# Kernel tuning notes

Measured on AMD Instinct MI355X. Metric: run time of the kernel, lower is better.

The kernel has to match this reference:

```python
import jax, jax.numpy as jnp
import numpy as np

V, D, G, E, B, S = 50000, 300, 256, 1600000, 64, 64


def setup_inputs() -> dict:
    key = jax.random.key(0)
    k = jax.random.split(key, 6)
    emb = jax.random.normal(k[0], (V, D), jnp.float32) * 0.02
    emb = emb.at[0].set(0.0)  # padding_idx=0
    W1 = jax.random.normal(k[1], (D, G), jnp.float32) * (1.0 / np.sqrt(D))
    b1 = jnp.zeros((G,), jnp.float32)
    W2 = jax.random.normal(k[2], (G, G), jnp.float32) * (1.0 / np.sqrt(G))
    b2 = jnp.zeros((G,), jnp.float32)
    edge_index = jax.random.randint(k[3], (2, E), 0, V, dtype=jnp.int64)
    word_ids = jax.random.randint(k[4], (B, S), 0, V, dtype=jnp.int64)
    return {"emb": emb, "W1": W1, "b1": b1, "W2": W2, "b2": b2,
            "edge_index": edge_index, "word_ids": word_ids}


def _gcn_conv(x, W, b, src, dst, num_nodes):
    """PyG GCNConv: add self-loops, symmetric deg^{-1/2} normalization.
    out_i = sum_{j->i} h_j / sqrt(deg_j * deg_i) + h_i / deg_i + b,
    with deg_i = 1 (self-loop) + in-degree(i), h = x @ W."""
    h = x @ W                                        # (N, G)
    deg = jnp.ones((num_nodes,), h.dtype).at[dst].add(1.0)
    inv_sqrt = jax.lax.rsqrt(deg)                    # (N,)
    coef = inv_sqrt[src] * inv_sqrt[dst]             # (E,)
    agg = jnp.zeros_like(h).at[dst].add(h[src] * coef[:, None])
    agg = agg + h * (inv_sqrt * inv_sqrt)[:, None]   # self-loop term
    return agg + b


def reference(emb, W1, b1, W2, b2, edge_index, word_ids):
    num_nodes = emb.shape[0]
    src, dst = edge_index[0], edge_index[1]
    h = jax.nn.relu(_gcn_conv(emb, W1, b1, src, dst, num_nodes))  # (V, G)
    h = _gcn_conv(h, W2, b2, src, dst, num_nodes)                 # (V, G)
    return h[word_ids]                                            # (B, S, G)
```

## Files before the change

kernel.cpp:

```cpp
#include <hip/hip_runtime.h>
#include <hip/hip_bf16.h>

#define NV 50000
#define ND 300
#define NDP 320
#define NG 256
#define NE 1600000
#define NBS 4096
#define NBUCK 196
#define EPB 8192
#define CPAD 16
#define GEMM1_BLOCKS 782
#define PREP_W1 320
#define PREP_W2 256
#define PREP_HIST 1024

typedef short short8 __attribute__((ext_vector_type(8)));
typedef float f32x4 __attribute__((ext_vector_type(4)));
typedef float f32x2 __attribute__((ext_vector_type(2)));
typedef _Float16 half4 __attribute__((ext_vector_type(4)));

__device__ __forceinline__ ushort f2bf(float f) {
    unsigned u = __builtin_bit_cast(unsigned, f);
    unsigned r = (u + 0x7fffu + ((u >> 16) & 1u)) >> 16;
    return (ushort)r;
}
__device__ __forceinline__ float bf2f(ushort h) {
    unsigned u = ((unsigned)h) << 16;
    return __builtin_bit_cast(float, u);
}

__global__ __launch_bounds__(256) void prep_kernel(const float* __restrict__ W1,
                                                   const float* __restrict__ W2,
                                                   ushort* __restrict__ W1Th,
                                                   ushort* __restrict__ W1Tl,
                                                   ushort* __restrict__ W2Th,
                                                   ushort* __restrict__ W2Tl,
                                                   const int* __restrict__ dst,
                                                   int* __restrict__ bucket_count) {
    int t = threadIdx.x;
    if (blockIdx.x < PREP_W1) {
        int idx = blockIdx.x * 256 + t;
        int n = idx / NDP, k = idx - n * NDP;
        float v = (k < ND) ? W1[(size_t)k * NG + n] : 0.f;
        ushort h = f2bf(v);
        W1Th[idx] = h;
        W1Tl[idx] = f2bf(v - bf2f(h));
    } else if (blockIdx.x < PREP_W1 + PREP_W2) {
        int j = (blockIdx.x - PREP_W1) * 256 + t;
        int n = j / NG, k = j - n * NG;
        float v = W2[(size_t)k * NG + n];
        ushort h = f2bf(v);
        W2Th[j] = h;
        W2Tl[j] = f2bf(v - bf2f(h));
    } else {
        __shared__ int bh[NBUCK];
        for (int b = t; b < NBUCK; b += 256) bh[b] = 0;
        __syncthreads();
        int blk = blockIdx.x - (PREP_W1 + PREP_W2);
        for (int i = blk * 256 + t; i * 4 < NE; i += PREP_HIST * 256) {
            int4 d = *(const int4*)(dst + i * 4);
            atomicAdd(&bh[d.x >> 8], 1);
            atomicAdd(&bh[d.y >> 8], 1);
            atomicAdd(&bh[d.z >> 8], 1);
            atomicAdd(&bh[d.w >> 8], 1);
        }
        __syncthreads();
        for (int b = t; b < NBUCK; b += 256)
            if (bh[b]) atomicAdd(&bucket_count[b * CPAD], bh[b]);
    }
}

__global__ __launch_bounds__(256) void bucket_scan(const int* __restrict__ bucket_count,
                                                   int* __restrict__ bucket_base,
                                                   int* __restrict__ bucket_cursor) {
    __shared__ int s[256];
    int t = threadIdx.x;
    int v = (t < NBUCK) ? bucket_count[t * CPAD] : 0;
    s[t] = v;
    __syncthreads();
    for (int d = 1; d < 256; d <<= 1) {
        int x = (t >= d) ? s[t - d] : 0;
        __syncthreads();
        s[t] += x;
        __syncthreads();
    }
    int excl = s[t] - v;
    if (t < NBUCK) {
        bucket_base[t] = excl;
        bucket_cursor[t * CPAD] = excl;
    }
    if (t == 255) bucket_base[NBUCK] = s[255];
}

__global__ __launch_bounds__(256) void gemm1_scatter(const float* __restrict__ A,
                                                     const ushort* __restrict__ BTh,
                                                     unsigned char* __restrict__ C8,
                                                     const int* __restrict__ ei,
                                                     int* __restrict__ bucket_cursor,
                                                     unsigned* __restrict__ rec) {
    int t = threadIdx.x;
    if (blockIdx.x < GEMM1_BLOCKS) {
        __shared__ short Ah[128][40];
        __shared__ short Bh[128][40];
        const int lda = ND, ldb = NDP, M = NV, K = ND, KP = NDP;
        int bid = blockIdx.x;
        int bm = (bid >> 1) * 128;
        int bn = (bid & 1) * 128;
        int lane = t & 63, wv = t >> 6;
        int wm = (wv >> 1) * 64, wn = (wv & 1) * 64;
        int srow = t >> 1;
        int skq = (t & 1) * 16;
        f32x4 acc[4][4];
#pragma unroll
        for (int mi = 0; mi < 4; ++mi)
#pragma unroll
            for (int ni = 0; ni < 4; ++ni) acc[mi][ni] = (f32x4)0.0f;

        for (int k0 = 0; k0 < KP; k0 += 32) {
            int gk = k0 + skq;
            {
                int gr = bm + srow;
                short va[16];
                float v[16];
                if (gr < M && gk < K) {
                    if (gk + 16 <= K) {
#pragma unroll
                        for (int q = 0; q < 4; ++q) {
                            float4 p = *(const float4*)(A + (size_t)gr * lda + gk + q * 4);
                            v[q * 4 + 0] = p.x; v[q * 4 + 1] = p.y;
                            v[q * 4 + 2] = p.z; v[q * 4 + 3] = p.w;
                        }
                    } else {
#pragma unroll
                        for (int e = 0; e < 16; ++e)
                            v[e] = (gk + e < K) ? A[(size_t)gr * lda + gk + e] : 0.f;
                    }
                } else {
#pragma unroll
                    for (int e = 0; e < 16; ++e) v[e] = 0.f;
                }
#pragma unroll
                for (int e = 0; e < 16; ++e) va[e] = (short)f2bf(v[e]);
                *(short8*)&Ah[srow][skq] = *(short8*)&va[0];
                *(short8*)&Ah[srow][skq + 8] = *(short8*)&va[8];
            }
            {
                int nr = bn + srow;
                short8 bh0 = *(const short8*)(BTh + (size_t)nr * ldb + gk);
                short8 bh1 = *(const short8*)(BTh + (size_t)nr * ldb + gk + 8);
                *(short8*)&Bh[srow][skq] = bh0;
                *(short8*)&Bh[srow][skq + 8] = bh1;
            }
            __syncthreads();
            int m16 = lane & 15, kb = (lane >> 4) * 8;
            short8 a_h[4], b_h[4];
#pragma unroll
            for (int mi = 0; mi < 4; ++mi)
                a_h[mi] = *(const short8*)&Ah[wm + mi * 16 + m16][kb];
#pragma unroll
            for (int ni = 0; ni < 4; ++ni)
                b_h[ni] = *(const short8*)&Bh[wn + ni * 16 + m16][kb];
#pragma unroll
            for (int mi = 0; mi < 4; ++mi)
#pragma unroll
                for (int ni = 0; ni < 4; ++ni)
                    acc[mi][ni] = __builtin_amdgcn_mfma_f32_16x16x32_bf16(a_h[mi], b_h[ni], acc[mi][ni], 0, 0, 0);
            __syncthreads();
        }
        int m16 = lane & 15, rq = lane >> 4;
#pragma unroll
        for (int mi = 0; mi < 4; ++mi)
#pragma unroll
            for (int ni = 0; ni < 4; ++ni) {
                int row0 = bm + wm + mi * 16 + rq * 4;
                int col = bn + wn + ni * 16 + m16;
                int p01 = __builtin_amdgcn_cvt_pk_fp8_f32(acc[mi][ni][0], acc[mi][ni][1], 0, false);
                int p23 = __builtin_amdgcn_cvt_pk_fp8_f32(acc[mi][ni][2], acc[mi][ni][3], 0, false);
                if (row0 + 0 < M) C8[(size_t)(row0 + 0) * NG + col] = (unsigned char)(p01 & 0xff);
                if (row0 + 1 < M) C8[(size_t)(row0 + 1) * NG + col] = (unsigned char)((p01 >> 8) & 0xff);
                if (row0 + 2 < M) C8[(size_t)(row0 + 2) * NG + col] = (unsigned char)(p23 & 0xff);
                if (row0 + 3 < M) C8[(size_t)(row0 + 3) * NG + col] = (unsigned char)((p23 >> 8) & 0xff);
            }
    } else {
        __shared__ int cnt[NBUCK];
        __shared__ int basel[NBUCK];
        int e0 = (blockIdx.x - GEMM1_BLOCKS) * EPB;
        for (int b = t; b < NBUCK; b += 256) cnt[b] = 0;
        __syncthreads();
        for (int q = 0; q < EPB / 1024; ++q) {
            int i4 = e0 + q * 1024 + t * 4;
            if (i4 < NE) {
                int4 d = *(const int4*)(ei + NE + i4);
                atomicAdd(&cnt[d.x >> 8], 1);
                atomicAdd(&cnt[d.y >> 8], 1);
                atomicAdd(&cnt[d.z >> 8], 1);
                atomicAdd(&cnt[d.w >> 8], 1);
            }
        }
        __syncthreads();
        for (int b = t; b < NBUCK; b += 256) {
            int c = cnt[b];
            basel[b] = c ? atomicAdd(&bucket_cursor[b * CPAD], c) : 0;
        }
        __syncthreads();
        for (int b = t; b < NBUCK; b += 256) cnt[b] = 0;
        __syncthreads();
        for (int q = 0; q < EPB / 1024; ++q) {
            int i4 = e0 + q * 1024 + t * 4;
            if (i4 < NE) {
                int4 s = *(const int4*)(ei + i4);
                int4 d = *(const int4*)(ei + NE + i4);
                int b0 = d.x >> 8, b1 = d.y >> 8, b2 = d.z >> 8, b3 = d.w >> 8;
                int r0 = atomicAdd(&cnt[b0], 1);
                rec[basel[b0] + r0] = (unsigned)s.x | ((unsigned)(d.x & 255) << 16);
                int r1 = atomicAdd(&cnt[b1], 1);
                rec[basel[b1] + r1] = (unsigned)s.y | ((unsigned)(d.y & 255) << 16);
                int r2 = atomicAdd(&cnt[b2], 1);
                rec[basel[b2] + r2] = (unsigned)s.z | ((unsigned)(d.z & 255) << 16);
                int r3 = atomicAdd(&cnt[b3], 1);
                rec[basel[b3] + r3] = (unsigned)s.w | ((unsigned)(d.w & 255) << 16);
            }
        }
    }
}

__global__ __launch_bounds__(256) void csr_build(const unsigned* __restrict__ rec,
                                                 const int* __restrict__ bucket_base,
                                                 int* __restrict__ off,
                                                 float* __restrict__ inv_sqrt,
                                                 ushort* __restrict__ csr_src) {
    __shared__ int degl[256];
    __shared__ int s[256];
    int b = blockIdx.x, t = threadIdx.x;
    degl[t] = 0;
    __syncthreads();
    int r0 = bucket_base[b], r1 = bucket_base[b + 1];
    for (int i = r0 + t; i < r1; i += 256)
        atomicAdd(&degl[(rec[i] >> 16) & 255], 1);
    __syncthreads();
    int v = degl[t];
    s[t] = v;
    __syncthreads();
    for (int d = 1; d < 256; d <<= 1) {
        int x = (t >= d) ? s[t - d] : 0;
        __syncthreads();
        s[t] += x;
        __syncthreads();
    }
    int excl = s[t] - v + r0;
    int n = (b << 8) + t;
    if (n < NV) {
        off[n] = excl;
        inv_sqrt[n] = rsqrtf((float)(v + 1));
    }
    if (b == NBUCK - 1 && t == 0) off[NV] = NE;
    __syncthreads();
    degl[t] = excl;
    __syncthreads();
    for (int i = r0 + t; i < r1; i += 256) {
        unsigned e = rec[i];
        int p = atomicAdd(&degl[(e >> 16) & 255], 1);
        csr_src[p] = (ushort)(e & 0xffff);
    }
}

__global__ __launch_bounds__(256) void gemm_out(const float* __restrict__ A,
                                                int lda,
                                                const ushort* __restrict__ BTh,
                                                const ushort* __restrict__ BTl,
                                                int ldb,
                                                int M, int K, int KP,
                                                float* __restrict__ C32,
                                                const float* __restrict__ bias) {
    __shared__ short Ah[128][40];
    __shared__ short Bh[128][40];
    __shared__ short Bl[128][40];
    int t = threadIdx.x;
    int bm = blockIdx.x * 128;
    int bn = blockIdx.y * 128;
    int lane = t & 63, wv = t >> 6;
    int wm = (wv >> 1) * 64, wn = (wv & 1) * 64;
    int srow = t >> 1;
    int skq = (t & 1) * 16;
    f32x4 acc[4][4];
#pragma unroll
    for (int mi = 0; mi < 4; ++mi)
#pragma unroll
        for (int ni = 0; ni < 4; ++ni) acc[mi][ni] = (f32x4)0.0f;

    for (int k0 = 0; k0 < KP; k0 += 32) {
        int gk = k0 + skq;
        {
            int gr = bm + srow;
            short va[16];
            float v[16];
            if (gr < M && gk < K) {
#pragma unroll
                for (int q = 0; q < 4; ++q) {
                    float4 p = *(const float4*)(A + (size_t)gr * lda + gk + q * 4);
                    v[q * 4 + 0] = p.x; v[q * 4 + 1] = p.y;
                    v[q * 4 + 2] = p.z; v[q * 4 + 3] = p.w;
                }
            } else {
#pragma unroll
                for (int e = 0; e < 16; ++e) v[e] = 0.f;
            }
#pragma unroll
            for (int e = 0; e < 16; ++e) va[e] = (short)f2bf(v[e]);
            *(short8*)&Ah[srow][skq] = *(short8*)&va[0];
            *(short8*)&Ah[srow][skq + 8] = *(short8*)&va[8];
        }
        {
            int nr = bn + srow;
            short8 bh0 = *(const short8*)(BTh + (size_t)nr * ldb + gk);
            short8 bh1 = *(const short8*)(BTh + (size_t)nr * ldb + gk + 8);
            short8 bl0 = *(const short8*)(BTl + (size_t)nr * ldb + gk);
            short8 bl1 = *(const short8*)(BTl + (size_t)nr * ldb + gk + 8);
            *(short8*)&Bh[srow][skq] = bh0;
            *(short8*)&Bh[srow][skq + 8] = bh1;
            *(short8*)&Bl[srow][skq] = bl0;
            *(short8*)&Bl[srow][skq + 8] = bl1;
        }
        __syncthreads();
        int m16 = lane & 15, kb = (lane >> 4) * 8;
        short8 a_h[4], b_h[4], b_l[4];
#pragma unroll
        for (int mi = 0; mi < 4; ++mi)
            a_h[mi] = *(const short8*)&Ah[wm + mi * 16 + m16][kb];
#pragma unroll
        for (int ni = 0; ni < 4; ++ni) {
            b_h[ni] = *(const short8*)&Bh[wn + ni * 16 + m16][kb];
            b_l[ni] = *(const short8*)&Bl[wn + ni * 16 + m16][kb];
        }
#pragma unroll
        for (int mi = 0; mi < 4; ++mi)
#pragma unroll
            for (int ni = 0; ni < 4; ++ni) {
                acc[mi][ni] = __builtin_amdgcn_mfma_f32_16x16x32_bf16(a_h[mi], b_h[ni], acc[mi][ni], 0, 0, 0);
                acc[mi][ni] = __builtin_amdgcn_mfma_f32_16x16x32_bf16(a_h[mi], b_l[ni], acc[mi][ni], 0, 0, 0);
            }
        __syncthreads();
    }
    int m16 = lane & 15, rq = lane >> 4;
#pragma unroll
    for (int mi = 0; mi < 4; ++mi)
#pragma unroll
        for (int ni = 0; ni < 4; ++ni) {
#pragma unroll
            for (int r = 0; r < 4; ++r) {
                int row = bm + wm + mi * 16 + rq * 4 + r;
                int col = bn + wn + ni * 16 + m16;
                if (row < M)
                    C32[(size_t)row * NG + col] = acc[mi][ni][r] + bias[col];
            }
        }
}

__global__ __launch_bounds__(256) void agg1_kernel(const unsigned char* __restrict__ h1f8,
                                                   const int* __restrict__ off,
                                                   const ushort* __restrict__ csr_src,
                                                   const float* __restrict__ inv_sqrt,
                                                   const float* __restrict__ b1,
                                                   _Float16* __restrict__ x1) {
    int wv = threadIdx.x >> 6, lane = threadIdx.x & 63;
    int i = blockIdx.x * 4 + wv;
    if (i >= NV) return;
    int c4 = lane * 4;
    int s0 = off[i], s1 = off[i + 1];
    float a0 = 0.f, a1 = 0.f, a2 = 0.f, a3 = 0.f;
    int j = s0;
    for (; j + 16 <= s1; j += 16) {
        int sx[16];
        float wx[16];
        unsigned pk[16];
#pragma unroll
        for (int u = 0; u < 16; ++u) sx[u] = csr_src[j + u];
#pragma unroll
        for (int u = 0; u < 16; ++u) {
            wx[u] = inv_sqrt[sx[u]];
            pk[u] = *(const unsigned*)(h1f8 + (size_t)sx[u] * NG + c4);
        }
#pragma unroll
        for (int u = 0; u < 16; ++u) {
            f32x2 v01 = __builtin_amdgcn_cvt_pk_f32_fp8(pk[u], false);
            f32x2 v23 = __builtin_amdgcn_cvt_pk_f32_fp8(pk[u], true);
            a0 += wx[u] * v01[0];
            a1 += wx[u] * v01[1];
            a2 += wx[u] * v23[0];
            a3 += wx[u] * v23[1];
        }
    }
    for (; j + 4 <= s1; j += 4) {
        int sx[4];
        float wx[4];
        unsigned pk[4];
#pragma unroll
        for (int u = 0; u < 4; ++u) sx[u] = csr_src[j + u];
#pragma unroll
        for (int u = 0; u < 4; ++u) {
            wx[u] = inv_sqrt[sx[u]];
            pk[u] = *(const unsigned*)(h1f8 + (size_t)sx[u] * NG + c4);
        }
#pragma unroll
        for (int u = 0; u < 4; ++u) {
            f32x2 v01 = __builtin_amdgcn_cvt_pk_f32_fp8(pk[u], false);
            f32x2 v23 = __builtin_amdgcn_cvt_pk_f32_fp8(pk[u], true);
            a0 += wx[u] * v01[0];
            a1 += wx[u] * v01[1];
            a2 += wx[u] * v23[0];
            a3 += wx[u] * v23[1];
        }
    }
    for (; j < s1; ++j) {
        int s = csr_src[j];
        float w = inv_sqrt[s];
        unsigned pk = *(const unsigned*)(h1f8 + (size_t)s * NG + c4);
        f32x2 v01 = __builtin_amdgcn_cvt_pk_f32_fp8(pk, false);
        f32x2 v23 = __builtin_amdgcn_cvt_pk_f32_fp8(pk, true);
        a0 += w * v01[0];
        a1 += w * v01[1];
        a2 += w * v23[0];
        a3 += w * v23[1];
    }
    float is = inv_sqrt[i], is2 = is * is;
    unsigned pks = *(const unsigned*)(h1f8 + (size_t)i * NG + c4);
    f32x2 s01 = __builtin_amdgcn_cvt_pk_f32_fp8(pks, false);
    f32x2 s23 = __builtin_amdgcn_cvt_pk_f32_fp8(pks, true);
    float4 bb = *(const float4*)(b1 + c4);
    half4 o;
    o[0] = (_Float16)fmaxf(is * a0 + s01[0] * is2 + bb.x, 0.f);
    o[1] = (_Float16)fmaxf(is * a1 + s01[1] * is2 + bb.y, 0.f);
    o[2] = (_Float16)fmaxf(is * a2 + s23[0] * is2 + bb.z, 0.f);
    o[3] = (_Float16)fmaxf(is * a3 + s23[1] * is2 + bb.w, 0.f);
    *(half4*)(x1 + (size_t)i * NG + c4) = o;
}

__global__ __launch_bounds__(256) void agg2_kernel(const _Float16* __restrict__ x1,
                                                   const int* __restrict__ off,
                                                   const ushort* __restrict__ csr_src,
                                                   const float* __restrict__ inv_sqrt,
                                                   const int* __restrict__ word_ids,
                                                   float* __restrict__ y) {
    int wv = threadIdx.x >> 6, lane = threadIdx.x & 63;
    int p = blockIdx.x * 4 + wv;
    if (p >= NBS) return;
    int n = word_ids[p];
    int c4 = lane * 4;
    int s0 = off[n], s1 = off[n + 1];
    float a0 = 0.f, a1 = 0.f, a2 = 0.f, a3 = 0.f;
    int j = s0;
    for (; j + 16 <= s1; j += 16) {
        int sx[16];
        float wx[16];
        half4 vx[16];
#pragma unroll
        for (int u = 0; u < 16; ++u) sx[u] = csr_src[j + u];
#pragma unroll
        for (int u = 0; u < 16; ++u) {
            wx[u] = inv_sqrt[sx[u]];
            vx[u] = *(const half4*)(x1 + (size_t)sx[u] * NG + c4);
        }
#pragma unroll
        for (int u = 0; u < 16; ++u) {
            a0 += wx[u] * (float)vx[u][0];
            a1 += wx[u] * (float)vx[u][1];
            a2 += wx[u] * (float)vx[u][2];
            a3 += wx[u] * (float)vx[u][3];
        }
    }
    for (; j + 4 <= s1; j += 4) {
        int sx[4];
        float wx[4];
        half4 vx[4];
#pragma unroll
        for (int u = 0; u < 4; ++u) sx[u] = csr_src[j + u];
#pragma unroll
        for (int u = 0; u < 4; ++u) {
            wx[u] = inv_sqrt[sx[u]];
            vx[u] = *(const half4*)(x1 + (size_t)sx[u] * NG + c4);
        }
#pragma unroll
        for (int u = 0; u < 4; ++u) {
            a0 += wx[u] * (float)vx[u][0];
            a1 += wx[u] * (float)vx[u][1];
            a2 += wx[u] * (float)vx[u][2];
            a3 += wx[u] * (float)vx[u][3];
        }
    }
    for (; j < s1; ++j) {
        int s = csr_src[j];
        float w = inv_sqrt[s];
        half4 hv = *(const half4*)(x1 + (size_t)s * NG + c4);
        a0 += w * (float)hv[0];
        a1 += w * (float)hv[1];
        a2 += w * (float)hv[2];
        a3 += w * (float)hv[3];
    }
    float is = inv_sqrt[n], is2 = is * is;
    half4 sv = *(const half4*)(x1 + (size_t)n * NG + c4);
    float4 o;
    o.x = is * a0 + (float)sv[0] * is2;
    o.y = is * a1 + (float)sv[1] * is2;
    o.z = is * a2 + (float)sv[2] * is2;
    o.w = is * a3 + (float)sv[3] * is2;
    *(float4*)(y + (size_t)p * NG + c4) = o;
}

extern "C" void kernel_launch(void* const* d_in, const int* in_sizes, int n_in,
                              void* d_out, int out_size, void* d_ws, size_t ws_size,
                              hipStream_t stream) {
    const float* emb = (const float*)d_in[0];
    const float* W1  = (const float*)d_in[1];
    const float* b1  = (const float*)d_in[2];
    const float* W2  = (const float*)d_in[3];
    const float* b2  = (const float*)d_in[4];
    const int*   ei  = (const int*)d_in[5];
    const int*   wid = (const int*)d_in[6];
    float* out = (float*)d_out;

    char* w = (char*)d_ws;
    auto alloc = [&](size_t bytes) {
        void* p = (void*)w;
        w += (bytes + 255) & ~(size_t)255;
        return p;
    };
    int*    off      = (int*)alloc((size_t)(NV + 1) * 4);
    float*  inv_sqrt = (float*)alloc((size_t)NV * 4);
    int*    bucket_count  = (int*)alloc((size_t)NBUCK * CPAD * 4);
    int*    bucket_base   = (int*)alloc((size_t)(NBUCK + 1) * 4);
    int*    bucket_cursor = (int*)alloc((size_t)NBUCK * CPAD * 4);
    ushort* csr_src  = (ushort*)alloc((size_t)NE * 2);
    unsigned* bucket_rec = (unsigned*)alloc((size_t)NE * 4);
    ushort* W1T_h    = (ushort*)alloc((size_t)NG * NDP * 2);
    ushort* W1T_l    = (ushort*)alloc((size_t)NG * NDP * 2);
    ushort* W2T_h    = (ushort*)alloc((size_t)NG * NG * 2);
    ushort* W2T_l    = (ushort*)alloc((size_t)NG * NG * 2);
    unsigned char* h1f8 = (unsigned char*)alloc((size_t)NV * NG);
    _Float16* x1     = (_Float16*)alloc((size_t)NV * NG * 2);
    float*  y        = (float*)alloc((size_t)NBS * NG * 4);

    hipMemsetAsync(bucket_count, 0, (size_t)NBUCK * CPAD * 4, stream);

    prep_kernel<<<PREP_W1 + PREP_W2 + PREP_HIST, 256, 0, stream>>>(
        W1, W2, W1T_h, W1T_l, W2T_h, W2T_l, ei + NE, bucket_count);
    bucket_scan<<<1, 256, 0, stream>>>(bucket_count, bucket_base, bucket_cursor);
    gemm1_scatter<<<GEMM1_BLOCKS + NBUCK, 256, 0, stream>>>(emb, W1T_h, h1f8,
                                                            ei, bucket_cursor, bucket_rec);
    csr_build<<<NBUCK, 256, 0, stream>>>(bucket_rec, bucket_base, off, inv_sqrt, csr_src);

    agg1_kernel<<<(NV + 3) / 4, 256, 0, stream>>>(h1f8, off, csr_src, inv_sqrt, b1, x1);
    agg2_kernel<<<(NBS + 3) / 4, 256, 0, stream>>>(x1, off, csr_src, inv_sqrt, wid, y);
    {
        dim3 grid((NBS + 127) / 128, NG / 128);
        gemm_out<<<grid, 256, 0, stream>>>(y, NG, W2T_h, W2T_l, NG,
                                           NBS, NG, NG, out, b2);
    }
}
```

Measured before the change: 191.5 us.

## Slice feature matrices into 32-column planes and aggregate per slice with lane groups

Hidden features h1 (fp8) and x1 (fp16) are now stored as eight column slices of 32 features each, with every slice contiguous over nodes. The aggregation kernels give each block one slice and split a wave into 8 edge groups of 8 lanes, then combine the groups with xor shuffles. The aim is to shrink each slice's working set so gathered rows stay in cache, and to run 8 edges in parallel per wave. The edge-scatter blocks are also placed ahead of the GEMM blocks with smaller per-block edge counts so they start early. The risks are extra shuffle reductions, 8x more blocks re-reading the CSR indices, and GEMM output stores that are scattered in the sliced layout.

```diff
diff --git a/kernel.cpp b/kernel.cpp
--- a/kernel.cpp
+++ b/kernel.cpp
@@ -8,7 +8,8 @@
 #define NE 1600000
 #define NBS 4096
 #define NBUCK 196
-#define EPB 8192
+#define EPB 4096
+#define SCAT_BLOCKS 391
 #define CPAD 16
 #define GEMM1_BLOCKS 782
 #define PREP_W1 320
@@ -95,97 +96,15 @@
 
 __global__ __launch_bounds__(256) void gemm1_scatter(const float* __restrict__ A,
                                                      const ushort* __restrict__ BTh,
-                                                     unsigned char* __restrict__ C8,
+                                                     unsigned char* __restrict__ h1s,
                                                      const int* __restrict__ ei,
                                                      int* __restrict__ bucket_cursor,
                                                      unsigned* __restrict__ rec) {
     int t = threadIdx.x;
-    if (blockIdx.x < GEMM1_BLOCKS) {
-        __shared__ short Ah[128][40];
-        __shared__ short Bh[128][40];
-        const int lda = ND, ldb = NDP, M = NV, K = ND, KP = NDP;
-        int bid = blockIdx.x;
-        int bm = (bid >> 1) * 128;
-        int bn = (bid & 1) * 128;
-        int lane = t & 63, wv = t >> 6;
-        int wm = (wv >> 1) * 64, wn = (wv & 1) * 64;
-        int srow = t >> 1;
-        int skq = (t & 1) * 16;
-        f32x4 acc[4][4];
-#pragma unroll
-        for (int mi = 0; mi < 4; ++mi)
-#pragma unroll
-            for (int ni = 0; ni < 4; ++ni) acc[mi][ni] = (f32x4)0.0f;
-
-        for (int k0 = 0; k0 < KP; k0 += 32) {
-            int gk = k0 + skq;
-            {
-                int gr = bm + srow;
-                short va[16];
-                float v[16];
-                if (gr < M && gk < K) {
-                    if (gk + 16 <= K) {
-#pragma unroll
-                        for (int q = 0; q < 4; ++q) {
-                            float4 p = *(const float4*)(A + (size_t)gr * lda + gk + q * 4);
-                            v[q * 4 + 0] = p.x; v[q * 4 + 1] = p.y;
-                            v[q * 4 + 2] = p.z; v[q * 4 + 3] = p.w;
-                        }
-                    } else {
-#pragma unroll
-                        for (int e = 0; e < 16; ++e)
-                            v[e] = (gk + e < K) ? A[(size_t)gr * lda + gk + e] : 0.f;
-                    }
-                } else {
-#pragma unroll
-                    for (int e = 0; e < 16; ++e) v[e] = 0.f;
-                }
-#pragma unroll
-                for (int e = 0; e < 16; ++e) va[e] = (short)f2bf(v[e]);
-                *(short8*)&Ah[srow][skq] = *(short8*)&va[0];
-                *(short8*)&Ah[srow][skq + 8] = *(short8*)&va[8];
-            }
-            {
-                int nr = bn + srow;
-                short8 bh0 = *(const short8*)(BTh + (size_t)nr * ldb + gk);
-                short8 bh1 = *(const short8*)(BTh + (size_t)nr * ldb + gk + 8);
-                *(short8*)&Bh[srow][skq] = bh0;
-                *(short8*)&Bh[srow][skq + 8] = bh1;
-            }
-            __syncthreads();
-            int m16 = lane & 15, kb = (lane >> 4) * 8;
-            short8 a_h[4], b_h[4];
-#pragma unroll
-            for (int mi = 0; mi < 4; ++mi)
-                a_h[mi] = *(const short8*)&Ah[wm + mi * 16 + m16][kb];
-#pragma unroll
-            for (int ni = 0; ni < 4; ++ni)
-                b_h[ni] = *(const short8*)&Bh[wn + ni * 16 + m16][kb];
-#pragma unroll
-            for (int mi = 0; mi < 4; ++mi)
-#pragma unroll
-                for (int ni = 0; ni < 4; ++ni)
-                    acc[mi][ni] = __builtin_amdgcn_mfma_f32_16x16x32_bf16(a_h[mi], b_h[ni], acc[mi][ni], 0, 0, 0);
-            __syncthreads();
-        }
-        int m16 = lane & 15, rq = lane >> 4;
-#pragma unroll
-        for (int mi = 0; mi < 4; ++mi)
-#pragma unroll
-            for (int ni = 0; ni < 4; ++ni) {
-                int row0 = bm + wm + mi * 16 + rq * 4;
-                int col = bn + wn + ni * 16 + m16;
-                int p01 = __builtin_amdgcn_cvt_pk_fp8_f32(acc[mi][ni][0], acc[mi][ni][1], 0, false);
-                int p23 = __builtin_amdgcn_cvt_pk_fp8_f32(acc[mi][ni][2], acc[mi][ni][3], 0, false);
-                if (row0 + 0 < M) C8[(size_t)(row0 + 0) * NG + col] = (unsigned char)(p01 & 0xff);
-                if (row0 + 1 < M) C8[(size_t)(row0 + 1) * NG + col] = (unsigned char)((p01 >> 8) & 0xff);
-                if (row0 + 2 < M) C8[(size_t)(row0 + 2) * NG + col] = (unsigned char)(p23 & 0xff);
-                if (row0 + 3 < M) C8[(size_t)(row0 + 3) * NG + col] = (unsigned char)((p23 >> 8) & 0xff);
-            }
-    } else {
+    if (blockIdx.x < SCAT_BLOCKS) {
         __shared__ int cnt[NBUCK];
         __shared__ int basel[NBUCK];
-        int e0 = (blockIdx.x - GEMM1_BLOCKS) * EPB;
+        int e0 = blockIdx.x * EPB;
         for (int b = t; b < NBUCK; b += 256) cnt[b] = 0;
         __syncthreads();
         for (int q = 0; q < EPB / 1024; ++q) {
@@ -222,6 +141,89 @@
                 rec[basel[b3] + r3] = (unsigned)s.w | ((unsigned)(d.w & 255) << 16);
             }
         }
+    } else {
+        __shared__ short Ah[128][40];
+        __shared__ short Bh[128][40];
+        const int lda = ND, ldb = NDP, M = NV, K = ND, KP = NDP;
+        int bid = blockIdx.x - SCAT_BLOCKS;
+        int bm = (bid >> 1) * 128;
+        int bn = (bid & 1) * 128;
+        int lane = t & 63, wv = t >> 6;
+        int wm = (wv >> 1) * 64, wn = (wv & 1) * 64;
+        int srow = t >> 1;
+        int skq = (t & 1) * 16;
+        f32x4 acc[4][4];
+#pragma unroll
+        for (int mi = 0; mi < 4; ++mi)
+#pragma unroll
+            for (int ni = 0; ni < 4; ++ni) acc[mi][ni] = (f32x4)0.0f;
+
+        for (int k0 = 0; k0 < KP; k0 += 32) {
+            int gk = k0 + skq;
+            {
+                int gr = bm + srow;
+                short va[16];
+                float v[16];
+                if (gr < M && gk < K) {
+                    if (gk + 16 <= K) {
+#pragma unroll
+                        for (int q = 0; q < 4; ++q) {
+                            float4 p = *(const float4*)(A + (size_t)gr * lda + gk + q * 4);
+                            v[q * 4 + 0] = p.x; v[q * 4 + 1] = p.y;
+                            v[q * 4 + 2] = p.z; v[q * 4 + 3] = p.w;
+                        }
+                    } else {
+#pragma unroll
+                        for (int e = 0; e < 16; ++e)
+                            v[e] = (gk + e < K) ? A[(size_t)gr * lda + gk + e] : 0.f;
+                    }
+                } else {
+#pragma unroll
+                    for (int e = 0; e < 16; ++e) v[e] = 0.f;
+                }
+#pragma unroll
+                for (int e = 0; e < 16; ++e) va[e] = (short)f2bf(v[e]);
+                *(short8*)&Ah[srow][skq] = *(short8*)&va[0];
+                *(short8*)&Ah[srow][skq + 8] = *(short8*)&va[8];
+            }
+            {
+                int nr = bn + srow;
+                short8 bh0 = *(const short8*)(BTh + (size_t)nr * ldb + gk);
+                short8 bh1 = *(const short8*)(BTh + (size_t)nr * ldb + gk + 8);
+                *(short8*)&Bh[srow][skq] = bh0;
+                *(short8*)&Bh[srow][skq + 8] = bh1;
+            }
+            __syncthreads();
+            int m16 = lane & 15, kb = (lane >> 4) * 8;
+            short8 a_h[4], b_h[4];
+#pragma unroll
+            for (int mi = 0; mi < 4; ++mi)
+                a_h[mi] = *(const short8*)&Ah[wm + mi * 16 + m16][kb];
+#pragma unroll
+            for (int ni = 0; ni < 4; ++ni)
+                b_h[ni] = *(const short8*)&Bh[wn + ni * 16 + m16][kb];
+#pragma unroll
+            for (int mi = 0; mi < 4; ++mi)
+#pragma unroll
+                for (int ni = 0; ni < 4; ++ni)
+                    acc[mi][ni] = __builtin_amdgcn_mfma_f32_16x16x32_bf16(a_h[mi], b_h[ni], acc[mi][ni], 0, 0, 0);
+            __syncthreads();
+        }
+        int m16 = lane & 15, rq = lane >> 4;
+#pragma unroll
+        for (int mi = 0; mi < 4; ++mi)
+#pragma unroll
+            for (int ni = 0; ni < 4; ++ni) {
+                int row0 = bm + wm + mi * 16 + rq * 4;
+                int col = bn + wn + ni * 16 + m16;
+                size_t base = (size_t)(col >> 5) * NV * 32 + (col & 31);
+                int p01 = __builtin_amdgcn_cvt_pk_fp8_f32(acc[mi][ni][0], acc[mi][ni][1], 0, false);
+                int p23 = __builtin_amdgcn_cvt_pk_fp8_f32(acc[mi][ni][2], acc[mi][ni][3], 0, false);
+                if (row0 + 0 < M) h1s[base + (size_t)(row0 + 0) * 32] = (unsigned char)(p01 & 0xff);
+                if (row0 + 1 < M) h1s[base + (size_t)(row0 + 1) * 32] = (unsigned char)((p01 >> 8) & 0xff);
+                if (row0 + 2 < M) h1s[base + (size_t)(row0 + 2) * 32] = (unsigned char)(p23 & 0xff);
+                if (row0 + 3 < M) h1s[base + (size_t)(row0 + 3) * 32] = (unsigned char)((p23 >> 8) & 0xff);
+            }
     }
 }
 
@@ -357,154 +359,133 @@
         }
 }
 
-__global__ __launch_bounds__(256) void agg1_kernel(const unsigned char* __restrict__ h1f8,
+__global__ __launch_bounds__(256) void agg1_kernel(const unsigned char* __restrict__ h1s,
                                                    const int* __restrict__ off,
                                                    const ushort* __restrict__ csr_src,
                                                    const float* __restrict__ inv_sqrt,
                                                    const float* __restrict__ b1,
-                                                   _Float16* __restrict__ x1) {
+                                                   _Float16* __restrict__ x1s) {
     int wv = threadIdx.x >> 6, lane = threadIdx.x & 63;
-    int i = blockIdx.x * 4 + wv;
-    if (i >= NV) return;
-    int c4 = lane * 4;
-    int s0 = off[i], s1 = off[i + 1];
-    float a0 = 0.f, a1 = 0.f, a2 = 0.f, a3 = 0.f;
-    int j = s0;
-    for (; j + 16 <= s1; j += 16) {
-        int sx[16];
-        float wx[16];
-        unsigned pk[16];
-#pragma unroll
-        for (int u = 0; u < 16; ++u) sx[u] = csr_src[j + u];
-#pragma unroll
-        for (int u = 0; u < 16; ++u) {
-            wx[u] = inv_sqrt[sx[u]];
-            pk[u] = *(const unsigned*)(h1f8 + (size_t)sx[u] * NG + c4);
-        }
-#pragma unroll
-        for (int u = 0; u < 16; ++u) {
-            f32x2 v01 = __builtin_amdgcn_cvt_pk_f32_fp8(pk[u], false);
-            f32x2 v23 = __builtin_amdgcn_cvt_pk_f32_fp8(pk[u], true);
-            a0 += wx[u] * v01[0];
-            a1 += wx[u] * v01[1];
-            a2 += wx[u] * v23[0];
-            a3 += wx[u] * v23[1];
-        }
-    }
-    for (; j + 4 <= s1; j += 4) {
-        int sx[4];
-        float wx[4];
-        unsigned pk[4];
-#pragma unroll
-        for (int u = 0; u < 4; ++u) sx[u] = csr_src[j + u];
-#pragma unroll
-        for (int u = 0; u < 4; ++u) {
-            wx[u] = inv_sqrt[sx[u]];
-            pk[u] = *(const unsigned*)(h1f8 + (size_t)sx[u] * NG + c4);
-        }
-#pragma unroll
-        for (int u = 0; u < 4; ++u) {
-            f32x2 v01 = __builtin_amdgcn_cvt_pk_f32_fp8(pk[u], false);
-            f32x2 v23 = __builtin_amdgcn_cvt_pk_f32_fp8(pk[u], true);
-            a0 += wx[u] * v01[0];
-            a1 += wx[u] * v01[1];
-            a2 += wx[u] * v23[0];
-            a3 += wx[u] * v23[1];
-        }
-    }
-    for (; j < s1; ++j) {
-        int s = csr_src[j];
-        float w = inv_sqrt[s];
-        unsigned pk = *(const unsigned*)(h1f8 + (size_t)s * NG + c4);
-        f32x2 v01 = __builtin_amdgcn_cvt_pk_f32_fp8(pk, false);
-        f32x2 v23 = __builtin_amdgcn_cvt_pk_f32_fp8(pk, true);
-        a0 += w * v01[0];
-        a1 += w * v01[1];
-        a2 += w * v23[0];
-        a3 += w * v23[1];
-    }
-    float is = inv_sqrt[i], is2 = is * is;
-    unsigned pks = *(const unsigned*)(h1f8 + (size_t)i * NG + c4);
-    f32x2 s01 = __builtin_amdgcn_cvt_pk_f32_fp8(pks, false);
-    f32x2 s23 = __builtin_amdgcn_cvt_pk_f32_fp8(pks, true);
-    float4 bb = *(const float4*)(b1 + c4);
-    half4 o;
-    o[0] = (_Float16)fmaxf(is * a0 + s01[0] * is2 + bb.x, 0.f);
-    o[1] = (_Float16)fmaxf(is * a1 + s01[1] * is2 + bb.y, 0.f);
-    o[2] = (_Float16)fmaxf(is * a2 + s23[0] * is2 + bb.z, 0.f);
-    o[3] = (_Float16)fmaxf(is * a3 + s23[1] * is2 + bb.w, 0.f);
-    *(half4*)(x1 + (size_t)i * NG + c4) = o;
-}
-
-__global__ __launch_bounds__(256) void agg2_kernel(const _Float16* __restrict__ x1,
+    int slice = blockIdx.x & 7;
+    int chunk = blockIdx.x >> 3;
+    int g = lane >> 3, p = lane & 7;
+    const unsigned char* hb = h1s + (size_t)slice * NV * 32;
+    _Float16* xb = x1s + (size_t)slice * NV * 32;
+    float4 bb = *(const float4*)(b1 + slice * 32 + p * 4);
+    for (int q = 0; q < 4; ++q) {
+        int i = chunk * 16 + wv * 4 + q;
+        if (i >= NV) break;
+        int s0 = off[i], s1 = off[i + 1];
+        float a0 = 0.f, a1 = 0.f, a2 = 0.f, a3 = 0.f;
+        int j = s0;
+        for (; j + 16 <= s1; j += 16) {
+            int sA = csr_src[j + g];
+            int sB = csr_src[j + 8 + g];
+            float wA = inv_sqrt[sA], wB = inv_sqrt[sB];
+            unsigned pA = *(const unsigned*)(hb + (size_t)sA * 32 + p * 4);
+            unsigned pB = *(const unsigned*)(hb + (size_t)sB * 32 + p * 4);
+            f32x2 vA01 = __builtin_amdgcn_cvt_pk_f32_fp8(pA, false);
+            f32x2 vA23 = __builtin_amdgcn_cvt_pk_f32_fp8(pA, true);
+            f32x2 vB01 = __builtin_amdgcn_cvt_pk_f32_fp8(pB, false);
+            f32x2 vB23 = __builtin_amdgcn_cvt_pk_f32_fp8(pB, true);
+            a0 += wA * vA01[0] + wB * vB01[0];
+            a1 += wA * vA01[1] + wB * vB01[1];
+            a2 += wA * vA23[0] + wB * vB23[0];
+            a3 += wA * vA23[1] + wB * vB23[1];
+        }
+        for (; j < s1; j += 8) {
+            int idx = j + g;
+            bool vld = idx < s1;
+            int sx = csr_src[vld ? idx : s0];
+            float w = vld ? inv_sqrt[sx] : 0.f;
+            unsigned pk = *(const unsigned*)(hb + (size_t)sx * 32 + p * 4);
+            f32x2 v01 = __builtin_amdgcn_cvt_pk_f32_fp8(pk, false);
+            f32x2 v23 = __builtin_amdgcn_cvt_pk_f32_fp8(pk, true);
+            a0 += w * v01[0];
+            a1 += w * v01[1];
+            a2 += w * v23[0];
+            a3 += w * v23[1];
+        }
+#pragma unroll
+        for (int d = 8; d < 64; d <<= 1) {
+            a0 += __shfl_xor(a0, d, 64);
+            a1 += __shfl_xor(a1, d, 64);
+            a2 += __shfl_xor(a2, d, 64);
+            a3 += __shfl_xor(a3, d, 64);
+        }
+        if (g == 0) {
+            float is = inv_sqrt[i], is2 = is * is;
+            unsigned pks = *(const unsigned*)(hb + (size_t)i * 32 + p * 4);
+            f32x2 s01 = __builtin_amdgcn_cvt_pk_f32_fp8(pks, false);
+            f32x2 s23 = __builtin_amdgcn_cvt_pk_f32_fp8(pks, true);
+            half4 o;
+            o[0] = (_Float16)fmaxf(is * a0 + s01[0] * is2 + bb.x, 0.f);
+            o[1] = (_Float16)fmaxf(is * a1 + s01[1] * is2 + bb.y, 0.f);
+            o[2] = (_Float16)fmaxf(is * a2 + s23[0] * is2 + bb.z, 0.f);
+            o[3] = (_Float16)fmaxf(is * a3 + s23[1] * is2 + bb.w, 0.f);
+            *(half4*)(xb + (size_t)i * 32 + p * 4) = o;
+        }
+    }
+}
+
+__global__ __launch_bounds__(256) void agg2_kernel(const _Float16* __restrict__ x1s,
                                                    const int* __restrict__ off,
                                                    const ushort* __restrict__ csr_src,
                                                    const float* __restrict__ inv_sqrt,
                                                    const int* __restrict__ word_ids,
                                                    float* __restrict__ y) {
     int wv = threadIdx.x >> 6, lane = threadIdx.x & 63;
-    int p = blockIdx.x * 4 + wv;
-    if (p >= NBS) return;
-    int n = word_ids[p];
-    int c4 = lane * 4;
-    int s0 = off[n], s1 = off[n + 1];
-    float a0 = 0.f, a1 = 0.f, a2 = 0.f, a3 = 0.f;
-    int j = s0;
-    for (; j + 16 <= s1; j += 16) {
-        int sx[16];
-        float wx[16];
-        half4 vx[16];
-#pragma unroll
-        for (int u = 0; u < 16; ++u) sx[u] = csr_src[j + u];
-#pragma unroll
-        for (int u = 0; u < 16; ++u) {
-            wx[u] = inv_sqrt[sx[u]];
-            vx[u] = *(const half4*)(x1 + (size_t)sx[u] * NG + c4);
-        }
-#pragma unroll
-        for (int u = 0; u < 16; ++u) {
-            a0 += wx[u] * (float)vx[u][0];
-            a1 += wx[u] * (float)vx[u][1];
-            a2 += wx[u] * (float)vx[u][2];
-            a3 += wx[u] * (float)vx[u][3];
-        }
-    }
-    for (; j + 4 <= s1; j += 4) {
-        int sx[4];
-        float wx[4];
-        half4 vx[4];
-#pragma unroll
-        for (int u = 0; u < 4; ++u) sx[u] = csr_src[j + u];
-#pragma unroll
-        for (int u = 0; u < 4; ++u) {
-            wx[u] = inv_sqrt[sx[u]];
-            vx[u] = *(const half4*)(x1 + (size_t)sx[u] * NG + c4);
-        }
-#pragma unroll
-        for (int u = 0; u < 4; ++u) {
-            a0 += wx[u] * (float)vx[u][0];
-            a1 += wx[u] * (float)vx[u][1];
-            a2 += wx[u] * (float)vx[u][2];
-            a3 += wx[u] * (float)vx[u][3];
-        }
-    }
-    for (; j < s1; ++j) {
-        int s = csr_src[j];
-        float w = inv_sqrt[s];
-        half4 hv = *(const half4*)(x1 + (size_t)s * NG + c4);
-        a0 += w * (float)hv[0];
-        a1 += w * (float)hv[1];
-        a2 += w * (float)hv[2];
-        a3 += w * (float)hv[3];
-    }
-    float is = inv_sqrt[n], is2 = is * is;
-    half4 sv = *(const half4*)(x1 + (size_t)n * NG + c4);
-    float4 o;
-    o.x = is * a0 + (float)sv[0] * is2;
-    o.y = is * a1 + (float)sv[1] * is2;
-    o.z = is * a2 + (float)sv[2] * is2;
-    o.w = is * a3 + (float)sv[3] * is2;
-    *(float4*)(y + (size_t)p * NG + c4) = o;
+    int slice = blockIdx.x & 7;
+    int chunk = blockIdx.x >> 3;
+    int g = lane >> 3, p = lane & 7;
+    const _Float16* xb = x1s + (size_t)slice * NV * 32;
+    for (int q = 0; q < 4; ++q) {
+        int pp = chunk * 16 + wv * 4 + q;
+        if (pp >= NBS) break;
+        int n = word_ids[pp];
+        int s0 = off[n], s1 = off[n + 1];
+        float a0 = 0.f, a1 = 0.f, a2 = 0.f, a3 = 0.f;
+        int j = s0;
+        for (; j + 16 <= s1; j += 16) {
+            int sA = csr_src[j + g];
+            int sB = csr_src[j + 8 + g];
+            float wA = inv_sqrt[sA], wB = inv_sqrt[sB];
+            half4 vA = *(const half4*)(xb + (size_t)sA * 32 + p * 4);
+            half4 vB = *(const half4*)(xb + (size_t)sB * 32 + p * 4);
+            a0 += wA * (float)vA[0] + wB * (float)vB[0];
+            a1 += wA * (float)vA[1] + wB * (float)vB[1];
+            a2 += wA * (float)vA[2] + wB * (float)vB[2];
+            a3 += wA * (float)vA[3] + wB * (float)vB[3];
+        }
+        for (; j < s1; j += 8) {
+            int idx = j + g;
+            bool vld = idx < s1;
+            int sx = csr_src[vld ? idx : s0];
+            float w = vld ? inv_sqrt[sx] : 0.f;
+            half4 hv = *(const half4*)(xb + (size_t)sx * 32 + p * 4);
+            a0 += w * (float)hv[0];
+            a1 += w * (float)hv[1];
+            a2 += w * (float)hv[2];
+            a3 += w * (float)hv[3];
+        }
+#pragma unroll
+        for (int d = 8; d < 64; d <<= 1) {
+            a0 += __shfl_xor(a0, d, 64);
+            a1 += __shfl_xor(a1, d, 64);
+            a2 += __shfl_xor(a2, d, 64);
+            a3 += __shfl_xor(a3, d, 64);
+        }
+        if (g == 0) {
+            float is = inv_sqrt[n], is2 = is * is;
+            half4 sv = *(const half4*)(xb + (size_t)n * 32 + p * 4);
+            float4 o;
+            o.x = is * a0 + (float)sv[0] * is2;
+            o.y = is * a1 + (float)sv[1] * is2;
+            o.z = is * a2 + (float)sv[2] * is2;
+            o.w = is * a3 + (float)sv[3] * is2;
+            *(float4*)(y + (size_t)pp * NG + slice * 32 + p * 4) = o;
+        }
+    }
 }
 
 extern "C" void kernel_launch(void* const* d_in, const int* in_sizes, int n_in,
@@ -536,8 +517,8 @@
     ushort* W1T_l    = (ushort*)alloc((size_t)NG * NDP * 2);
     ushort* W2T_h    = (ushort*)alloc((size_t)NG * NG * 2);
     ushort* W2T_l    = (ushort*)alloc((size_t)NG * NG * 2);
-    unsigned char* h1f8 = (unsigned char*)alloc((size_t)NV * NG);
-    _Float16* x1     = (_Float16*)alloc((size_t)NV * NG * 2);
+    unsigned char* h1s = (unsigned char*)alloc((size_t)NV * NG);
+    _Float16* x1s    = (_Float16*)alloc((size_t)NV * NG * 2);
     float*  y        = (float*)alloc((size_t)NBS * NG * 4);
 
     hipMemsetAsync(bucket_count, 0, (size_t)NBUCK * CPAD * 4, stream);
@@ -545,12 +526,12 @@
     prep_kernel<<<PREP_W1 + PREP_W2 + PREP_HIST, 256, 0, stream>>>(
         W1, W2, W1T_h, W1T_l, W2T_h, W2T_l, ei + NE, bucket_count);
     bucket_scan<<<1, 256, 0, stream>>>(bucket_count, bucket_base, bucket_cursor);
-    gemm1_scatter<<<GEMM1_BLOCKS + NBUCK, 256, 0, stream>>>(emb, W1T_h, h1f8,
-                                                            ei, bucket_cursor, bucket_rec);
+    gemm1_scatter<<<SCAT_BLOCKS + GEMM1_BLOCKS, 256, 0, stream>>>(emb, W1T_h, h1s,
+                                                                  ei, bucket_cursor, bucket_rec);
     csr_build<<<NBUCK, 256, 0, stream>>>(bucket_rec, bucket_base, off, inv_sqrt, csr_src);
 
-    agg1_kernel<<<(NV + 3) / 4, 256, 0, stream>>>(h1f8, off, csr_src, inv_sqrt, b1, x1);
-    agg2_kernel<<<(NBS + 3) / 4, 256, 0, stream>>>(x1, off, csr_src, inv_sqrt, wid, y);
+    agg1_kernel<<<(NV / 16) * 8, 256, 0, stream>>>(h1s, off, csr_src, inv_sqrt, b1, x1s);
+    agg2_kernel<<<(NBS / 16) * 8, 256, 0, stream>>>(x1s, off, csr_src, inv_sqrt, wid, y);
     {
         dim3 grid((NBS + 127) / 128, NG / 128);
         gemm_out<<<grid, 256, 0, stream>>>(y, NG, W2T_h, W2T_l, NG,
```

New measurement: 271.7 us. 41.9% more time.
